# Optimization experiments

Hardware: AMD Instinct MI355X
Metric: run time of the kernel (lower is better)

## Reference

```python
import jax, jax.numpy as jnp
import numpy as np

TOP_K = 2  # matches init_kwargs top_k


def setup_inputs() -> dict:
    key = jax.random.key(0)
    ks = jax.random.split(key, 8)
    B, S, D, E, H = 4, 2048, 1024, 8, 4096
    scale = lambda fan_in: 1.0 / np.sqrt(fan_in)
    return {
        "x": jax.random.normal(ks[0], (B, S, D), jnp.float32),
        "noise": jax.random.normal(ks[1], (B, S, E), jnp.float32),
        "Wg": jax.random.normal(ks[2], (D, E), jnp.float32) * scale(D),
        "bg": jnp.zeros((E,), jnp.float32),
        "Wn": jax.random.normal(ks[3], (D, E), jnp.float32) * scale(D),
        "bn": jnp.zeros((E,), jnp.float32),
        "W1": jax.random.normal(ks[4], (E, D, H), jnp.float32) * scale(D),
        "b1": jnp.zeros((E, H), jnp.float32),
        "W2": jax.random.normal(ks[5], (E, H, D), jnp.float32) * scale(H),
        "b2": jnp.zeros((E, D), jnp.float32),
    }


def reference(x, noise, Wg, bg, Wn, bn, W1, b1, W2, b2):
    B, S, D = x.shape
    E = Wg.shape[1]
    t = x.reshape(-1, D)            # [T, D] flat tokens
    n = noise.reshape(-1, E)        # [T, E]

    # NoisyTopK router
    logits = t @ Wg + bg                                  # [T, E]
    noise_logits = t @ Wn + bn                            # [T, E]
    noisy = logits + n * jax.nn.softplus(noise_logits)    # [T, E]
    _, idx = jax.lax.top_k(noisy, TOP_K)                  # [T, K] expert ids
    sel = jax.nn.one_hot(idx, E, dtype=jnp.bool_).any(-2) # [T, E] selected mask
    # scatter topk logits into -inf, softmax -> zeros at unselected experts
    gate = jax.nn.softmax(jnp.where(sel, noisy, -jnp.inf), axis=-1)  # [T, E]

    # per-expert dense FFN + weighted combine (gate is exactly 0 off top-k)
    out = jnp.zeros_like(t)
    for e in range(E):
        h = jax.nn.relu(t @ W1[e] + b1[e])  # [T, H]
        y = h @ W2[e] + b2[e]               # [T, D]
        w = jnp.where(sel[:, e], gate[:, e], 0.0)[:, None]
        out = out + w * y
    return out.reshape(B, S, D)
```

## Files before the change

kernel.cpp:

```cpp
#include <hip/hip_runtime.h>
#include <math.h>

#define TOPK 2

using bf16x8 = __attribute__((ext_vector_type(8))) short;
using f32x4  = __attribute__((ext_vector_type(4))) float;

__device__ __forceinline__ unsigned short f2bf(float f) {
    unsigned int u = __float_as_uint(f);
    u += 0x7fffu + ((u >> 16) & 1u);
    return (unsigned short)(u >> 16);
}
__device__ __forceinline__ float bf2f(unsigned short s) {
    return __uint_as_float(((unsigned int)s) << 16);
}

__device__ __forceinline__ void async_copy16(const void* g, void* l) {
    __builtin_amdgcn_global_load_lds(
        (const __attribute__((address_space(1))) unsigned int*)g,
        (__attribute__((address_space(3))) unsigned int*)l, 16, 0, 0);
}

template<int E>
__global__ __launch_bounds__(64) void router_kernel(
    const float* __restrict__ x, const float* __restrict__ noise,
    const float* __restrict__ Wg, const float* __restrict__ bg,
    const float* __restrict__ Wn, const float* __restrict__ bn,
    int T, int D,
    int* __restrict__ count, int* __restrict__ topk_e, float* __restrict__ topk_g)
{
    int t = blockIdx.x;
    int lane = threadIdx.x;
    float ag[E], an[E];
#pragma unroll
    for (int e = 0; e < E; ++e) { ag[e] = 0.f; an[e] = 0.f; }
    const float* xrow = x + (size_t)t * D;
    for (int d = lane; d < D; d += 64) {
        float xv = xrow[d];
        const float* wgr = Wg + (size_t)d * E;
        const float* wnr = Wn + (size_t)d * E;
#pragma unroll
        for (int e = 0; e < E; ++e) {
            ag[e] = fmaf(xv, wgr[e], ag[e]);
            an[e] = fmaf(xv, wnr[e], an[e]);
        }
    }
#pragma unroll
    for (int e = 0; e < E; ++e) {
#pragma unroll
        for (int off = 32; off; off >>= 1) {
            ag[e] += __shfl_xor(ag[e], off, 64);
            an[e] += __shfl_xor(an[e], off, 64);
        }
    }
    if (lane == 0) {
        float noisy[E];
#pragma unroll
        for (int e = 0; e < E; ++e) {
            float lg = ag[e] + bg[e];
            float nl = an[e] + bn[e];
            float sp = fmaxf(nl, 0.f) + log1pf(expf(-fabsf(nl)));
            noisy[e] = lg + noise[(size_t)t * E + e] * sp;
        }
        int e0 = 0; float v0 = noisy[0];
#pragma unroll
        for (int e = 1; e < E; ++e) if (noisy[e] > v0) { v0 = noisy[e]; e0 = e; }
        int e1 = -1; float v1 = -INFINITY;
#pragma unroll
        for (int e = 0; e < E; ++e) if (e != e0 && noisy[e] > v1) { v1 = noisy[e]; e1 = e; }
        float d1 = expf(v1 - v0);
        float g0 = 1.f / (1.f + d1);
        float g1 = d1 / (1.f + d1);
        topk_e[2 * t] = e0; topk_e[2 * t + 1] = e1;
        topk_g[2 * t] = g0; topk_g[2 * t + 1] = g1;
        atomicAdd(&count[e0], 1);
        atomicAdd(&count[e1], 1);
    }
}

__global__ void scan_kernel(const int* __restrict__ count, int* __restrict__ offsets, int E)
{
    if (threadIdx.x == 0 && blockIdx.x == 0) {
        int acc = 0;
        for (int e = 0; e < E; ++e) { offsets[e] = acc; acc += count[e]; }
        offsets[E] = acc;
    }
}

__global__ void scatter_kernel(
    const int* __restrict__ topk_e, const float* __restrict__ topk_g,
    const int* __restrict__ offsets, int* __restrict__ fill,
    int* __restrict__ rows, float* __restrict__ rgate, int T)
{
    int t = blockIdx.x * blockDim.x + threadIdx.x;
    if (t >= T) return;
#pragma unroll
    for (int k = 0; k < TOPK; ++k) {
        int e = topk_e[2 * t + k];
        int slot = atomicAdd(&fill[e], 1);
        int p = offsets[e] + slot;
        rows[p] = t;
        rgate[p] = topk_g[2 * t + k];
    }
}

__global__ void split_x_kernel(const float* __restrict__ x,
                               unsigned short* __restrict__ xh,
                               unsigned short* __restrict__ xl, size_t n4)
{
    size_t i = (size_t)blockIdx.x * blockDim.x + threadIdx.x;
    if (i >= n4) return;
    float4 v = ((const float4*)x)[i];
    ushort4 h, l;
    h.x = f2bf(v.x); l.x = f2bf(v.x - bf2f(h.x));
    h.y = f2bf(v.y); l.y = f2bf(v.y - bf2f(h.y));
    h.z = f2bf(v.z); l.z = f2bf(v.z - bf2f(h.z));
    h.w = f2bf(v.w); l.w = f2bf(v.w - bf2f(h.w));
    ((ushort4*)xh)[i] = h;
    ((ushort4*)xl)[i] = l;
}

__global__ __launch_bounds__(256) void transpose_split_kernel(
    const float* __restrict__ src, size_t sE, int srow0, int ld_s, int scol0,
    unsigned short* __restrict__ dh, unsigned short* __restrict__ dl,
    size_t dE, int ld_d)
{
    const int e  = blockIdx.z;
    const int n0 = blockIdx.x * 32;
    const int k0 = blockIdx.y * 32;
    const int tx = threadIdx.x & 31;
    const int ty = threadIdx.x >> 5;
    __shared__ float tile[32][33];
    const float* s = src + (size_t)e * sE;
#pragma unroll
    for (int p = 0; p < 4; ++p) {
        int k = k0 + ty + 8 * p;
        tile[ty + 8 * p][tx] = s[(size_t)(srow0 + k) * ld_s + scol0 + n0 + tx];
    }
    __syncthreads();
    unsigned short* oh = dh + (size_t)e * dE;
    unsigned short* ol = dl + (size_t)e * dE;
#pragma unroll
    for (int p = 0; p < 4; ++p) {
        int n = n0 + ty + 8 * p;
        float v = tile[tx][ty + 8 * p];
        unsigned short h = f2bf(v);
        unsigned short l = f2bf(v - bf2f(h));
        size_t o = (size_t)n * ld_d + k0 + tx;
        oh[o] = h; ol[o] = l;
    }
}

template<int MODE>
__global__ __launch_bounds__(256, 2) void moe_gemm(
    const short* __restrict__ Agh, const short* __restrict__ Agl,
    const short* __restrict__ Bgh, const short* __restrict__ Bgl,
    size_t Bes,
    const float* __restrict__ bias,
    const int* __restrict__ count, const int* __restrict__ offsets,
    const int* __restrict__ rows, const float* __restrict__ rgate,
    unsigned short* __restrict__ Oh, unsigned short* __restrict__ Ol,
    float* __restrict__ out,
    int lda, int K, int Hc, int H, int D, int hc0, int addb2)
{
    const int e   = blockIdx.z;
    const int cnt = count[e];
    const int m0  = blockIdx.y * 128;
    if (m0 >= cnt) return;
    const int base = offsets[e];
    const int n0   = blockIdx.x * 128;

    const int tid  = threadIdx.x;
    const int wid  = tid >> 6;
    const int lane = tid & 63;
    const int wm   = wid >> 1;
    const int wn   = wid & 1;

    __shared__ __align__(16) short sAh[128 * 32];
    __shared__ __align__(16) short sAl[128 * 32];
    __shared__ __align__(16) short sBh[128 * 32];
    __shared__ __align__(16) short sBl[128 * 32];

    const int r2 = tid >> 2;
    const int cs = (tid & 3) ^ ((r2 >> 1) & 3);

    int mA0 = m0 + r2;      if (mA0 >= cnt) mA0 = cnt - 1;
    int mA1 = m0 + 64 + r2; if (mA1 >= cnt) mA1 = cnt - 1;
    size_t ar0, ar1;
    if (MODE == 1) { ar0 = (size_t)rows[base + mA0]; ar1 = (size_t)rows[base + mA1]; }
    else           { ar0 = (size_t)(base + mA0);     ar1 = (size_t)(base + mA1); }

    const short* pAh0 = Agh + ar0 * lda + cs * 8;
    const short* pAh1 = Agh + ar1 * lda + cs * 8;
    const short* pAl0 = Agl + ar0 * lda + cs * 8;
    const short* pAl1 = Agl + ar1 * lda + cs * 8;

    const size_t be = (size_t)e * Bes;
    const short* pBh0 = Bgh + be + (size_t)(n0 + r2) * K + cs * 8;
    const short* pBh1 = Bgh + be + (size_t)(n0 + 64 + r2) * K + cs * 8;
    const short* pBl0 = Bgl + be + (size_t)(n0 + r2) * K + cs * 8;
    const short* pBl1 = Bgl + be + (size_t)(n0 + 64 + r2) * K + cs * 8;

    const int lm = lane & 15;
    const int kq = lane >> 4;

    f32x4 acc[4][4];
#pragma unroll
    for (int i = 0; i < 4; ++i)
#pragma unroll
        for (int j = 0; j < 4; ++j)
            acc[i][j] = (f32x4){0.f, 0.f, 0.f, 0.f};

    int offA[4], offB[4];
#pragma unroll
    for (int f = 0; f < 4; ++f) {
        int ra = wm * 64 + f * 16 + lm;
        offA[f] = ra * 32 + (kq ^ ((ra >> 1) & 3)) * 8;
        int rb = wn * 64 + f * 16 + lm;
        offB[f] = rb * 32 + (kq ^ ((rb >> 1) & 3)) * 8;
    }

    for (int k0 = 0; k0 < K; k0 += 32) {
        async_copy16(pAh0 + k0, sAh + tid * 8);
        async_copy16(pAh1 + k0, sAh + (256 + tid) * 8);
        async_copy16(pAl0 + k0, sAl + tid * 8);
        async_copy16(pAl1 + k0, sAl + (256 + tid) * 8);
        async_copy16(pBh0 + k0, sBh + tid * 8);
        async_copy16(pBh1 + k0, sBh + (256 + tid) * 8);
        async_copy16(pBl0 + k0, sBl + tid * 8);
        async_copy16(pBl1 + k0, sBl + (256 + tid) * 8);
        __syncthreads();

        bf16x8 ah[4], al[4], bh[4], bl[4];
#pragma unroll
        for (int f = 0; f < 4; ++f) {
            ah[f] = *(const bf16x8*)(sAh + offA[f]);
            al[f] = *(const bf16x8*)(sAl + offA[f]);
            bh[f] = *(const bf16x8*)(sBh + offB[f]);
            bl[f] = *(const bf16x8*)(sBl + offB[f]);
        }
#pragma unroll
        for (int i = 0; i < 4; ++i)
#pragma unroll
            for (int j = 0; j < 4; ++j) {
                acc[i][j] = __builtin_amdgcn_mfma_f32_16x16x32_bf16(ah[i], bh[j], acc[i][j], 0, 0, 0);
                acc[i][j] = __builtin_amdgcn_mfma_f32_16x16x32_bf16(ah[i], bl[j], acc[i][j], 0, 0, 0);
                acc[i][j] = __builtin_amdgcn_mfma_f32_16x16x32_bf16(al[i], bh[j], acc[i][j], 0, 0, 0);
            }
        __syncthreads();
    }

    if (MODE == 1) {
#pragma unroll
        for (int j = 0; j < 4; ++j) {
            const int nc = n0 + wn * 64 + j * 16 + lm;
            const float bv = bias[(size_t)e * H + hc0 + nc];
#pragma unroll
            for (int i = 0; i < 4; ++i) {
#pragma unroll
                for (int r = 0; r < 4; ++r) {
                    const int m = m0 + wm * 64 + i * 16 + kq * 4 + r;
                    if (m < cnt) {
                        float v = fmaxf(acc[i][j][r] + bv, 0.f);
                        unsigned short h = f2bf(v);
                        unsigned short l = f2bf(v - bf2f(h));
                        size_t o = (size_t)(base + m) * Hc + nc;
                        Oh[o] = h; Ol[o] = l;
                    }
                }
            }
        }
    } else {
#pragma unroll
        for (int i = 0; i < 4; ++i) {
#pragma unroll
            for (int r = 0; r < 4; ++r) {
                const int m = m0 + wm * 64 + i * 16 + kq * 4 + r;
                if (m < cnt) {
                    const int t = rows[base + m];
                    const float g = rgate[base + m];
                    float* orow = out + (size_t)t * D;
#pragma unroll
                    for (int j = 0; j < 4; ++j) {
                        const int nc = n0 + wn * 64 + j * 16 + lm;
                        float v = acc[i][j][r];
                        if (addb2) v += bias[(size_t)e * D + nc];
                        atomicAdd(orow + nc, g * v);
                    }
                }
            }
        }
    }
}

extern "C" void kernel_launch(void* const* d_in, const int* in_sizes, int n_in,
                              void* d_out, int out_size, void* d_ws, size_t ws_size,
                              hipStream_t stream)
{
    const float* x     = (const float*)d_in[0];
    const float* noise = (const float*)d_in[1];
    const float* Wg    = (const float*)d_in[2];
    const float* bg    = (const float*)d_in[3];
    const float* Wn    = (const float*)d_in[4];
    const float* bn    = (const float*)d_in[5];
    const float* W1    = (const float*)d_in[6];
    const float* b1    = (const float*)d_in[7];
    const float* W2    = (const float*)d_in[8];
    const float* b2    = (const float*)d_in[9];

    const int E = in_sizes[3];
    const int D = in_sizes[2] / E;
    const int T = in_sizes[0] / D;
    const int H = in_sizes[7] / E;
    const int T2 = 2 * T;
    float* out = (float*)d_out;

    char* p = (char*)d_ws;
    auto alloc = [&](size_t bytes) -> char* {
        char* r = p; p += (bytes + 255) & ~(size_t)255; return r;
    };

    int*   count   = (int*)alloc(256);
    int*   fill    = (int*)alloc(256);
    int*   offsets = (int*)alloc(256);
    int*   topk_e  = (int*)alloc((size_t)T2 * 4);
    float* topk_g  = (float*)alloc((size_t)T2 * 4);
    int*   rows    = (int*)alloc((size_t)T2 * 4);
    float* rgate   = (float*)alloc((size_t)T2 * 4);
    unsigned short* xh = (unsigned short*)alloc((size_t)T * D * 2);
    unsigned short* xl = (unsigned short*)alloc((size_t)T * D * 2);

    const size_t fixed = (size_t)(p - (char*)d_ws);
    auto pad = [](size_t b) { return (b + 255) & ~(size_t)255; };
    int Hc = 128;
    for (int c = H; c >= 128; c >>= 1) {
        if (H % c) continue;
        size_t need = fixed
            + 2 * pad((size_t)E * c * D * 2)
            + 2 * pad((size_t)E * D * c * 2)
            + 2 * pad((size_t)T2 * c * 2);
        if (need <= ws_size) { Hc = c; break; }
    }
    unsigned short* w1h = (unsigned short*)alloc((size_t)E * Hc * D * 2);
    unsigned short* w1l = (unsigned short*)alloc((size_t)E * Hc * D * 2);
    unsigned short* w2h = (unsigned short*)alloc((size_t)E * D * Hc * 2);
    unsigned short* w2l = (unsigned short*)alloc((size_t)E * D * Hc * 2);
    unsigned short* hbh = (unsigned short*)alloc((size_t)T2 * Hc * 2);
    unsigned short* hbl = (unsigned short*)alloc((size_t)T2 * Hc * 2);

    hipMemsetAsync(d_ws, 0, 768, stream);
    hipMemsetAsync(d_out, 0, (size_t)out_size * 4, stream);

    if (E == 8) {
        router_kernel<8><<<T, 64, 0, stream>>>(x, noise, Wg, bg, Wn, bn, T, D,
                                               count, topk_e, topk_g);
    } else if (E == 16) {
        router_kernel<16><<<T, 64, 0, stream>>>(x, noise, Wg, bg, Wn, bn, T, D,
                                                count, topk_e, topk_g);
    } else {
        router_kernel<4><<<T, 64, 0, stream>>>(x, noise, Wg, bg, Wn, bn, T, D,
                                               count, topk_e, topk_g);
    }
    scan_kernel<<<1, 64, 0, stream>>>(count, offsets, E);
    scatter_kernel<<<(T + 255) / 256, 256, 0, stream>>>(topk_e, topk_g, offsets, fill,
                                                        rows, rgate, T);
    split_x_kernel<<<((T * D / 4) + 255) / 256, 256, 0, stream>>>(
        x, xh, xl, (size_t)T * D / 4);

    const int nTm = (T + 127) / 128;
    for (int hc0 = 0; hc0 < H; hc0 += Hc) {
        transpose_split_kernel<<<dim3(Hc / 32, D / 32, E), 256, 0, stream>>>(
            W1, (size_t)D * H, 0, H, hc0, w1h, w1l, (size_t)Hc * D, D);
        transpose_split_kernel<<<dim3(D / 32, Hc / 32, E), 256, 0, stream>>>(
            W2, (size_t)H * D, hc0, D, 0, w2h, w2l, (size_t)D * Hc, Hc);

        moe_gemm<1><<<dim3(Hc / 128, nTm, E), 256, 0, stream>>>(
            (const short*)xh, (const short*)xl, (const short*)w1h, (const short*)w1l,
            (size_t)Hc * D, b1, count, offsets, rows, rgate,
            hbh, hbl, nullptr, D, D, Hc, H, D, hc0, 0);

        moe_gemm<2><<<dim3(D / 128, nTm, E), 256, 0, stream>>>(
            (const short*)hbh, (const short*)hbl, (const short*)w2h, (const short*)w2l,
            (size_t)D * Hc, b2, count, offsets, rows, rgate,
            nullptr, nullptr, out, Hc, Hc, Hc, H, D, hc0, hc0 == 0 ? 1 : 0);
    }
}
```

Measured before the change: 1.748 ms.

## Double-buffer GEMM LDS tiles and widen transpose-split stores to packed pairs

The MoE GEMM now keeps two LDS buffers and issues the async global-to-LDS loads for the next K-slice before computing the current one, with a single barrier per iteration. This is meant to overlap memory latency with MFMA work. It doubles LDS use to 64KB per block, which may reduce occupancy below the declared two blocks per CU. Separately, the weight transpose/split kernel handles 64 K-rows per block and writes two bf16 values per 32-bit store, cutting the number of store instructions.

Measured after the change: 1.806 ms. 1.03x slower.

```diff
diff --git a/kernel.cpp b/kernel.cpp
--- a/kernel.cpp
+++ b/kernel.cpp
@@ -126,28 +126,31 @@
     size_t dE, int ld_d)
 {
     const int e  = blockIdx.z;
+    const int k0 = blockIdx.y * 64;
     const int n0 = blockIdx.x * 32;
-    const int k0 = blockIdx.y * 32;
-    const int tx = threadIdx.x & 31;
-    const int ty = threadIdx.x >> 5;
-    __shared__ float tile[32][33];
-    const float* s = src + (size_t)e * sE;
+    const int tn = threadIdx.x & 31;
+    const int tk = threadIdx.x >> 5;
+    __shared__ float tile[64][33];
+    const float* s = src + (size_t)e * sE + (size_t)(srow0 + k0) * ld_s + scol0 + n0;
+#pragma unroll
+    for (int p = 0; p < 8; ++p)
+        tile[tk + 8 * p][tn] = s[(size_t)(tk + 8 * p) * ld_s + tn];
+    __syncthreads();
+    const int kk = (threadIdx.x & 31) * 2;
+    const int ny = threadIdx.x >> 5;
+    unsigned int* oh = (unsigned int*)(dh + (size_t)e * dE);
+    unsigned int* ol = (unsigned int*)(dl + (size_t)e * dE);
 #pragma unroll
     for (int p = 0; p < 4; ++p) {
-        int k = k0 + ty + 8 * p;
-        tile[ty + 8 * p][tx] = s[(size_t)(srow0 + k) * ld_s + scol0 + n0 + tx];
-    }
-    __syncthreads();
-    unsigned short* oh = dh + (size_t)e * dE;
-    unsigned short* ol = dl + (size_t)e * dE;
-#pragma unroll
-    for (int p = 0; p < 4; ++p) {
-        int n = n0 + ty + 8 * p;
-        float v = tile[tx][ty + 8 * p];
-        unsigned short h = f2bf(v);
-        unsigned short l = f2bf(v - bf2f(h));
-        size_t o = (size_t)n * ld_d + k0 + tx;
-        oh[o] = h; ol[o] = l;
+        int nl_ = ny + 8 * p;
+        int n = n0 + nl_;
+        float v0 = tile[kk][nl_];
+        float v1 = tile[kk + 1][nl_];
+        unsigned short h0 = f2bf(v0), h1 = f2bf(v1);
+        unsigned short l0 = f2bf(v0 - bf2f(h0)), l1 = f2bf(v1 - bf2f(h1));
+        size_t o = ((size_t)n * ld_d + k0 + kk) >> 1;
+        oh[o] = (unsigned int)h0 | ((unsigned int)h1 << 16);
+        ol[o] = (unsigned int)l0 | ((unsigned int)l1 << 16);
     }
 }
 
@@ -176,10 +179,7 @@
     const int wm   = wid >> 1;
     const int wn   = wid & 1;
 
-    __shared__ __align__(16) short sAh[128 * 32];
-    __shared__ __align__(16) short sAl[128 * 32];
-    __shared__ __align__(16) short sBh[128 * 32];
-    __shared__ __align__(16) short sBl[128 * 32];
+    __shared__ __align__(16) short sm[2][4][128 * 32];
 
     const int r2 = tid >> 2;
     const int cs = (tid & 3) ^ ((r2 >> 1) & 3);
@@ -220,16 +220,27 @@
         offB[f] = rb * 32 + (kq ^ ((rb >> 1) & 3)) * 8;
     }
 
-    for (int k0 = 0; k0 < K; k0 += 32) {
-        async_copy16(pAh0 + k0, sAh + tid * 8);
-        async_copy16(pAh1 + k0, sAh + (256 + tid) * 8);
-        async_copy16(pAl0 + k0, sAl + tid * 8);
-        async_copy16(pAl1 + k0, sAl + (256 + tid) * 8);
-        async_copy16(pBh0 + k0, sBh + tid * 8);
-        async_copy16(pBh1 + k0, sBh + (256 + tid) * 8);
-        async_copy16(pBl0 + k0, sBl + tid * 8);
-        async_copy16(pBl1 + k0, sBl + (256 + tid) * 8);
+    auto stage = [&](int b, int k0) {
+        async_copy16(pAh0 + k0, &sm[b][0][tid * 8]);
+        async_copy16(pAh1 + k0, &sm[b][0][(256 + tid) * 8]);
+        async_copy16(pAl0 + k0, &sm[b][1][tid * 8]);
+        async_copy16(pAl1 + k0, &sm[b][1][(256 + tid) * 8]);
+        async_copy16(pBh0 + k0, &sm[b][2][tid * 8]);
+        async_copy16(pBh1 + k0, &sm[b][2][(256 + tid) * 8]);
+        async_copy16(pBl0 + k0, &sm[b][3][tid * 8]);
+        async_copy16(pBl1 + k0, &sm[b][3][(256 + tid) * 8]);
+    };
+
+    const int nt = K >> 5;
+    stage(0, 0);
+    for (int t = 0; t < nt; ++t) {
         __syncthreads();
+        if (t + 1 < nt) stage((t + 1) & 1, (t + 1) << 5);
+
+        const short* sAh = &sm[t & 1][0][0];
+        const short* sAl = &sm[t & 1][1][0];
+        const short* sBh = &sm[t & 1][2][0];
+        const short* sBl = &sm[t & 1][3][0];
 
         bf16x8 ah[4], al[4], bh[4], bl[4];
 #pragma unroll
@@ -247,7 +258,6 @@
                 acc[i][j] = __builtin_amdgcn_mfma_f32_16x16x32_bf16(ah[i], bl[j], acc[i][j], 0, 0, 0);
                 acc[i][j] = __builtin_amdgcn_mfma_f32_16x16x32_bf16(al[i], bh[j], acc[i][j], 0, 0, 0);
             }
-        __syncthreads();
     }
 
     if (MODE == 1) {
@@ -369,9 +379,9 @@
 
     const int nTm = (T + 127) / 128;
     for (int hc0 = 0; hc0 < H; hc0 += Hc) {
-        transpose_split_kernel<<<dim3(Hc / 32, D / 32, E), 256, 0, stream>>>(
+        transpose_split_kernel<<<dim3(Hc / 32, D / 64, E), 256, 0, stream>>>(
             W1, (size_t)D * H, 0, H, hc0, w1h, w1l, (size_t)Hc * D, D);
-        transpose_split_kernel<<<dim3(D / 32, Hc / 32, E), 256, 0, stream>>>(
+        transpose_split_kernel<<<dim3(D / 32, Hc / 64, E), 256, 0, stream>>>(
             W2, (size_t)H * D, hc0, D, 0, w2h, w2l, (size_t)D * Hc, Hc);
 
         moe_gemm<1><<<dim3(Hc / 128, nTm, E), 256, 0, stream>>>(
```
